# Optimization experiments

Measured on AMD Instinct MI355X. Metric: run time of the kernel, lower is better.

The kernel has to match this reference:

```python
import jax, jax.numpy as jnp
import numpy as np

N = 50000
D = 256
S = 25  # num_samples


def setup_inputs() -> dict:
    key = jax.random.key(0)
    ks = jax.random.split(key, 8)
    sc = 1.0 / np.sqrt(D)
    sc2 = 1.0 / np.sqrt(2 * D)
    return {
        "features": jax.random.normal(ks[0], (N, D), dtype=jnp.float32),
        "neigh_idx": jax.random.randint(ks[1], (N, S), 0, N, dtype=jnp.int64),
        "Wp0": jax.random.normal(ks[2], (D, D), dtype=jnp.float32) * sc,
        "bp0": jnp.zeros((D,), dtype=jnp.float32),
        "Wfc0": jax.random.normal(ks[3], (2 * D, D), dtype=jnp.float32) * sc2,
        "bfc0": jnp.zeros((D,), dtype=jnp.float32),
        "Wp1": jax.random.normal(ks[4], (D, D), dtype=jnp.float32) * sc,
        "bp1": jnp.zeros((D,), dtype=jnp.float32),
        "Wfc1": jax.random.normal(ks[5], (2 * D, D), dtype=jnp.float32) * sc2,
        "bfc1": jnp.zeros((D,), dtype=jnp.float32),
    }


def _sage_layer(out, neigh_idx, Wp, bp, Wfc, bfc):
    # MaxPoolAggregator: per-node Linear+ReLU on neighbor feats, then max-pool.
    # Transform once over all nodes, then gather (same math, less traffic).
    h = jax.nn.relu(out @ Wp + bp)          # [N, d]
    agg = jnp.max(h[neigh_idx], axis=1)     # gather [N, S, d] -> max -> [N, d]
    cat = jnp.concatenate([out, agg], axis=1)  # [N, 2d]
    return cat @ Wfc + bfc                  # [N, hidden]


def reference(features, neigh_idx, Wp0, bp0, Wfc0, bfc0, Wp1, bp1, Wfc1, bfc1):
    out = _sage_layer(features, neigh_idx, Wp0, bp0, Wfc0, bfc0)
    out = jax.nn.relu(out)  # relu between layers; dropout(p=0) is a no-op
    out = _sage_layer(out, neigh_idx, Wp1, bp1, Wfc1, bfc1)
    return out
```

## Files before the change

kernel.cpp:

```cpp
#include <hip/hip_runtime.h>
#include <stdint.h>

#define N_NODES 50000
#define DD 256
#define SS 25

typedef unsigned short u16;
typedef __attribute__((ext_vector_type(8))) __bf16 bf16x8;
typedef __attribute__((ext_vector_type(4))) float f32x4;

__device__ __forceinline__ u16 f2bf(float f) {
    union { float f; uint32_t i; } c;
    c.f = f;
    uint32_t r = c.i + 0x7fffu + ((c.i >> 16) & 1u);
    return (u16)(r >> 16);
}

__device__ __forceinline__ uint4 pkmax4(uint4 a, uint4 b) {
    uint4 d;
    asm("v_pk_max_i16 %0, %1, %2" : "=v"(d.x) : "v"(a.x), "v"(b.x));
    asm("v_pk_max_i16 %0, %1, %2" : "=v"(d.y) : "v"(a.y), "v"(b.y));
    asm("v_pk_max_i16 %0, %1, %2" : "=v"(d.z) : "v"(a.z), "v"(b.z));
    asm("v_pk_max_i16 %0, %1, %2" : "=v"(d.w) : "v"(a.w), "v"(b.w));
    return d;
}

__device__ __forceinline__ void gld16(void* lds, const void* g) {
    __builtin_amdgcn_global_load_lds(
        (const __attribute__((address_space(1))) uint32_t*)g,
        (__attribute__((address_space(3))) uint32_t*)lds, 16, 0, 0);
}

__global__ __launch_bounds__(256) void cvt_f32_bf16_k(const float4* __restrict__ in,
                                                      u16* __restrict__ out) {
    int i = blockIdx.x * 256 + threadIdx.x;
    float4 v = in[i];
    uint2 o;
    o.x = (uint32_t)f2bf(v.x) | ((uint32_t)f2bf(v.y) << 16);
    o.y = (uint32_t)f2bf(v.z) | ((uint32_t)f2bf(v.w) << 16);
    *reinterpret_cast<uint2*>(out + (size_t)i * 4) = o;
}

__global__ __launch_bounds__(256) void cvt_w_k(const float* __restrict__ W,
                                               u16* __restrict__ out, int KT) {
    int t = blockIdx.x * 256 + threadIdx.x;
    if (t >= KT * 16 * 64) return;
    int lane = t & 63;
    int ct = (t >> 6) & 15;
    int kt = t >> 10;
    int k0 = kt * 32 + (lane >> 4) * 8;
    int col = ct * 16 + (lane & 15);
    u16 r[8];
#pragma unroll
    for (int e = 0; e < 8; e++) r[e] = f2bf(W[(size_t)(k0 + e) * DD + col]);
    uint4 v;
    v.x = (uint32_t)r[0] | ((uint32_t)r[1] << 16);
    v.y = (uint32_t)r[2] | ((uint32_t)r[3] << 16);
    v.z = (uint32_t)r[4] | ((uint32_t)r[5] << 16);
    v.w = (uint32_t)r[6] | ((uint32_t)r[7] << 16);
    *reinterpret_cast<uint4*>(out + (size_t)t * 8) = v;
}

__global__ __launch_bounds__(256) void gather_xcd_k(const u16* __restrict__ hc,
                                                    const int* __restrict__ idx,
                                                    u16* __restrict__ aggc, int M) {
    const int c = blockIdx.x & 7;
    const int base = (blockIdx.x >> 3) * 256;
    __shared__ int soff[256 * SS];
    const int tid = threadIdx.x;
    for (int j = tid; j < 256 * SS; j += 256) {
        int n = base + j / SS;
        if (n >= M) n = M - 1;
        soff[j] = idx[(size_t)n * SS + (j % SS)] * 32;
    }
    __syncthreads();
    const int q = tid & 3;
    const u16* slice = hc + (size_t)c * ((size_t)N_NODES * 32) + q * 8;
    u16* aslice = aggc + (size_t)c * ((size_t)N_NODES * 32) + q * 8;
#pragma unroll 1
    for (int p = 0; p < 4; ++p) {
        const int slot = p * 64 + (tid >> 2);
        const int n = base + slot;
        const int* off = &soff[slot * SS];
        uint4 v[13];
#pragma unroll
        for (int s = 0; s < 13; ++s)
            v[s] = *reinterpret_cast<const uint4*>(slice + off[s]);
        uint4 run = v[0];
#pragma unroll
        for (int s = 1; s < 13; ++s) run = pkmax4(run, v[s]);
#pragma unroll
        for (int s = 13; s < 25; ++s)
            v[s - 13] = *reinterpret_cast<const uint4*>(slice + off[s]);
#pragma unroll
        for (int s = 0; s < 12; ++s) run = pkmax4(run, v[s]);
        if (n < M)
            *reinterpret_cast<uint4*>(aslice + (size_t)n * 32) = run;
    }
}

template <int KT, bool RELU, int OMODE>
__global__ __launch_bounds__(512, 4) void gemm_k(const u16* __restrict__ A1,
                                                 const u16* __restrict__ A2,
                                                 const u16* __restrict__ Bf,
                                                 const float* __restrict__ bias,
                                                 u16* __restrict__ obf,
                                                 float* __restrict__ of32, int M) {
    __shared__ u16 sA[4][4096];
    __shared__ u16 sB[3][8192];
    const int tid = threadIdx.x;
    const int lane = tid & 63, w = tid >> 6;
    const int wm = w >> 2, wn = w & 3;
    const int row_base = blockIdx.x * 128;
    const int lr = lane & 15, lk = lane >> 4;

    const int arow = tid >> 2;
    const int swzr = (arow + (arow >> 2)) & 3;
    const int kc = (tid & 3) ^ swzr;
    int sgrow = row_base + arow;
    if (sgrow >= M) sgrow = M - 1;

    auto stageB = [&](int buf, int kt) {
#pragma unroll
        for (int j = 0; j < 2; ++j) {
            const int idx = tid + j * 512;
            const int nl = idx >> 6, li = idx & 63;
            gld16(&sB[buf][idx * 8], Bf + ((size_t)(kt * 16 + nl) * 64 + li) * 8);
        }
    };
    auto stageA = [&](int buf, int kt) {
        const u16* srcA = (KT == 16 && kt >= 8)
                              ? A2 + ((size_t)(kt & 7) * N_NODES + sgrow) * 32 + kc * 8
                              : A1 + (size_t)sgrow * DD + (kt & 7) * 32 + kc * 8;
        gld16(&sA[buf][tid * 8], srcA);
    };

    f32x4 acc[4][4] = {};
    const int swzl = (lr + (lr >> 2)) & 3;
    auto compute = [&](int bufA, int bufB) {
        bf16x8 a[4], b[4];
#pragma unroll
        for (int m = 0; m < 4; m++) {
            const int row = wm * 64 + m * 16 + lr;
            a[m] = *reinterpret_cast<const bf16x8*>(
                &sA[bufA][(row * 4 + (lk ^ swzl)) * 8]);
        }
#pragma unroll
        for (int n = 0; n < 4; n++)
            b[n] = *reinterpret_cast<const bf16x8*>(
                &sB[bufB][((wn * 4 + n) * 64 + lane) * 8]);
#pragma unroll
        for (int m = 0; m < 4; m++)
#pragma unroll
            for (int n = 0; n < 4; n++)
                acc[m][n] = __builtin_amdgcn_mfma_f32_16x16x32_bf16(a[m], b[n], acc[m][n], 0, 0, 0);
    };

    stageB(0, 0);
    stageA(0, 0);
    stageB(1, 1);
    stageA(1, 1);
    stageA(2, 2);
#pragma unroll
    for (int kt = 0; kt < KT; ++kt) {
        if (kt < KT - 2)
            asm volatile("s_waitcnt vmcnt(4)" ::: "memory");
        else if (kt == KT - 2)
            asm volatile("s_waitcnt vmcnt(3)" ::: "memory");
        else
            asm volatile("s_waitcnt vmcnt(0)" ::: "memory");
        __builtin_amdgcn_s_barrier();
        if (kt + 2 < KT) stageB((kt + 2) % 3, kt + 2);
        if (kt + 3 < KT) stageA((kt + 3) & 3, kt + 3);
        compute(kt & 3, kt % 3);
    }

#pragma unroll
    for (int n = 0; n < 4; n++) {
        const int col = wn * 64 + n * 16 + lr;
        const float bz = bias[col];
#pragma unroll
        for (int m = 0; m < 4; m++) {
            const int r0 = row_base + wm * 64 + m * 16 + lk * 4;
#pragma unroll
            for (int e = 0; e < 4; e++) {
                const int r = r0 + e;
                if (r < M) {
                    float v = acc[m][n][e] + bz;
                    if (RELU) v = fmaxf(v, 0.0f);
                    if (OMODE == 0)
                        obf[(size_t)r * DD + col] = f2bf(v);
                    else if (OMODE == 1)
                        obf[((size_t)(col >> 5) * N_NODES + r) * 32 + (col & 31)] = f2bf(v);
                    else
                        of32[(size_t)r * DD + col] = v;
                }
            }
        }
    }
}

extern "C" void kernel_launch(void* const* d_in, const int* in_sizes, int n_in,
                              void* d_out, int out_size, void* d_ws, size_t ws_size,
                              hipStream_t stream) {
    const float* features = (const float*)d_in[0];
    const int* neigh = (const int*)d_in[1];
    const float* Wp0 = (const float*)d_in[2];
    const float* bp0 = (const float*)d_in[3];
    const float* Wfc0 = (const float*)d_in[4];
    const float* bfc0 = (const float*)d_in[5];
    const float* Wp1 = (const float*)d_in[6];
    const float* bp1 = (const float*)d_in[7];
    const float* Wfc1 = (const float*)d_in[8];
    const float* bfc1 = (const float*)d_in[9];
    float* out = (float*)d_out;

    const size_t ND = (size_t)N_NODES * DD;
    u16* B0 = (u16*)d_ws;
    u16* B1 = B0 + ND;
    u16* B2 = B1 + ND;
    u16* Wpb0 = B2 + ND;
    u16* Wfb0 = Wpb0 + 65536;
    u16* Wpb1 = Wfb0 + 131072;
    u16* Wfb1 = Wpb1 + 65536;

    cvt_w_k<<<32, 256, 0, stream>>>(Wp0, Wpb0, 8);
    cvt_w_k<<<64, 256, 0, stream>>>(Wfc0, Wfb0, 16);
    cvt_w_k<<<32, 256, 0, stream>>>(Wp1, Wpb1, 8);
    cvt_w_k<<<64, 256, 0, stream>>>(Wfc1, Wfb1, 16);
    cvt_f32_bf16_k<<<12500, 256, 0, stream>>>((const float4*)features, B0);

    const int gg = (N_NODES + 127) / 128;
    const int gx = ((N_NODES + 255) / 256) * 8;

    gemm_k<8, true, 1><<<gg, 512, 0, stream>>>(B0, nullptr, Wpb0, bp0, B1, nullptr, N_NODES);
    gather_xcd_k<<<gx, 256, 0, stream>>>(B1, neigh, B2, N_NODES);
    gemm_k<16, true, 0><<<gg, 512, 0, stream>>>(B0, B2, Wfb0, bfc0, B1, nullptr, N_NODES);

    gemm_k<8, true, 1><<<gg, 512, 0, stream>>>(B1, nullptr, Wpb1, bp1, B0, nullptr, N_NODES);
    gather_xcd_k<<<gx, 256, 0, stream>>>(B0, neigh, B2, N_NODES);
    gemm_k<16, false, 2><<<gg, 512, 0, stream>>>(B1, B2, Wfb1, bfc1, nullptr, out, N_NODES);
}
```

Baseline: 221.9 us.

## Fuse layer-0 FC GEMM with layer-1 pool projection GEMM in one kernel

Adds a kernel that computes the layer-0 concat FC (relu) for a 128-row tile, writes it to global, then immediately reuses the same block to compute the layer-1 pool projection from those rows. The intermediate is stored in the output buffer (bf16, column-blocked layout) to serve as the gather source. This removes one kernel launch and is meant to let the second GEMM re-read freshly written rows while they are still in cache. The trade-off is a longer kernel with reduced parallel overlap, and a read-after-write through global memory within the block that relies on a waitcnt and barrier for visibility.

```diff
diff --git a/kernel.cpp b/kernel.cpp
--- a/kernel.cpp
+++ b/kernel.cpp
@@ -200,6 +200,152 @@
     }
 }
 
+__global__ __launch_bounds__(512, 4) void fused2_k(const u16* __restrict__ X,
+                                                   const u16* __restrict__ agg0,
+                                                   const u16* __restrict__ BfT,
+                                                   const float* __restrict__ b0,
+                                                   u16* __restrict__ O0,
+                                                   const u16* __restrict__ Bp1,
+                                                   const float* __restrict__ b1,
+                                                   u16* __restrict__ h1c,
+                                                   int M) {
+    __shared__ u16 sA[4][4096];
+    __shared__ u16 sB[3][8192];
+    const int tid = threadIdx.x;
+    const int lane = tid & 63, w = tid >> 6;
+    const int wm = w >> 2, wn = w & 3;
+    const int row_base = blockIdx.x * 128;
+    const int lr = lane & 15, lk = lane >> 4;
+
+    const int arow = tid >> 2;
+    const int swzr = (arow + (arow >> 2)) & 3;
+    const int kc = (tid & 3) ^ swzr;
+    int sgrow = row_base + arow;
+    if (sgrow >= M) sgrow = M - 1;
+
+    const int swzl = (lr + (lr >> 2)) & 3;
+
+    auto stageB = [&](const u16* Bf, int buf, int kt) {
+#pragma unroll
+        for (int j = 0; j < 2; ++j) {
+            const int idx = tid + j * 512;
+            const int nl = idx >> 6, li = idx & 63;
+            gld16(&sB[buf][idx * 8], Bf + ((size_t)(kt * 16 + nl) * 64 + li) * 8);
+        }
+    };
+    auto stageA1 = [&](const u16* A1, int buf, int kt) {
+        gld16(&sA[buf][tid * 8], A1 + (size_t)sgrow * DD + (kt & 7) * 32 + kc * 8);
+    };
+    auto stageA2 = [&](const u16* A2, int buf, int kt) {
+        gld16(&sA[buf][tid * 8], A2 + ((size_t)(kt & 7) * N_NODES + sgrow) * 32 + kc * 8);
+    };
+
+    f32x4 acc[4][4] = {};
+    auto compute = [&](int bufA, int bufB) {
+        bf16x8 a[4], b[4];
+#pragma unroll
+        for (int m = 0; m < 4; m++) {
+            const int row = wm * 64 + m * 16 + lr;
+            a[m] = *reinterpret_cast<const bf16x8*>(
+                &sA[bufA][(row * 4 + (lk ^ swzl)) * 8]);
+        }
+#pragma unroll
+        for (int n = 0; n < 4; n++)
+            b[n] = *reinterpret_cast<const bf16x8*>(
+                &sB[bufB][((wn * 4 + n) * 64 + lane) * 8]);
+#pragma unroll
+        for (int m = 0; m < 4; m++)
+#pragma unroll
+            for (int n = 0; n < 4; n++)
+                acc[m][n] = __builtin_amdgcn_mfma_f32_16x16x32_bf16(a[m], b[n], acc[m][n], 0, 0, 0);
+    };
+
+    stageB(BfT, 0, 0);
+    stageA1(X, 0, 0);
+    stageB(BfT, 1, 1);
+    stageA1(X, 1, 1);
+    stageA1(X, 2, 2);
+#pragma unroll
+    for (int kt = 0; kt < 16; ++kt) {
+        if (kt < 14)
+            asm volatile("s_waitcnt vmcnt(4)" ::: "memory");
+        else if (kt == 14)
+            asm volatile("s_waitcnt vmcnt(3)" ::: "memory");
+        else
+            asm volatile("s_waitcnt vmcnt(0)" ::: "memory");
+        __builtin_amdgcn_s_barrier();
+        if (kt + 2 < 16) stageB(BfT, (kt + 2) % 3, kt + 2);
+        if (kt + 3 < 16) {
+            if (kt + 3 < 8)
+                stageA1(X, (kt + 3) & 3, kt + 3);
+            else
+                stageA2(agg0, (kt + 3) & 3, kt + 3);
+        }
+        compute(kt & 3, kt % 3);
+    }
+
+#pragma unroll
+    for (int n = 0; n < 4; n++) {
+        const int col = wn * 64 + n * 16 + lr;
+        const float bz = b0[col];
+#pragma unroll
+        for (int m = 0; m < 4; m++) {
+            const int r0 = row_base + wm * 64 + m * 16 + lk * 4;
+#pragma unroll
+            for (int e = 0; e < 4; e++) {
+                const int r = r0 + e;
+                if (r < M) O0[(size_t)r * DD + col] = f2bf(fmaxf(acc[m][n][e] + bz, 0.0f));
+            }
+        }
+    }
+    asm volatile("s_waitcnt vmcnt(0)" ::: "memory");
+    __builtin_amdgcn_s_barrier();
+
+#pragma unroll
+    for (int m = 0; m < 4; m++)
+#pragma unroll
+        for (int n = 0; n < 4; n++) acc[m][n] = f32x4{0.f, 0.f, 0.f, 0.f};
+
+    stageB(Bp1, 0, 0);
+    stageB(Bp1, 1, 1);
+    stageA1(O0, 0, 0);
+    stageA1(O0, 1, 1);
+    stageA1(O0, 2, 2);
+#pragma unroll
+    for (int kt = 0; kt < 8; ++kt) {
+        if (kt == 0)
+            asm volatile("s_waitcnt vmcnt(2)" ::: "memory");
+        else if (kt < 6)
+            asm volatile("s_waitcnt vmcnt(4)" ::: "memory");
+        else if (kt == 6)
+            asm volatile("s_waitcnt vmcnt(3)" ::: "memory");
+        else
+            asm volatile("s_waitcnt vmcnt(0)" ::: "memory");
+        __builtin_amdgcn_s_barrier();
+        if (kt + 2 < 8) stageB(Bp1, (kt + 2) % 3, kt + 2);
+        if (kt + 3 < 8) stageA1(O0, (kt + 3) & 3, kt + 3);
+        compute(kt & 3, kt % 3);
+    }
+
+#pragma unroll
+    for (int n = 0; n < 4; n++) {
+        const int col = wn * 64 + n * 16 + lr;
+        const float bz = b1[col];
+#pragma unroll
+        for (int m = 0; m < 4; m++) {
+            const int r0 = row_base + wm * 64 + m * 16 + lk * 4;
+#pragma unroll
+            for (int e = 0; e < 4; e++) {
+                const int r = r0 + e;
+                if (r < M) {
+                    float v = fmaxf(acc[m][n][e] + bz, 0.0f);
+                    h1c[((size_t)(col >> 5) * N_NODES + r) * 32 + (col & 31)] = f2bf(v);
+                }
+            }
+        }
+    }
+}
+
 extern "C" void kernel_launch(void* const* d_in, const int* in_sizes, int n_in,
                               void* d_out, int out_size, void* d_ws, size_t ws_size,
                               hipStream_t stream) {
@@ -223,6 +369,7 @@
     u16* Wfb0 = Wpb0 + 65536;
     u16* Wpb1 = Wfb0 + 131072;
     u16* Wfb1 = Wpb1 + 65536;
+    u16* H1 = (u16*)d_out;
 
     cvt_w_k<<<32, 256, 0, stream>>>(Wp0, Wpb0, 8);
     cvt_w_k<<<64, 256, 0, stream>>>(Wfc0, Wfb0, 16);
@@ -235,9 +382,8 @@
 
     gemm_k<8, true, 1><<<gg, 512, 0, stream>>>(B0, nullptr, Wpb0, bp0, B1, nullptr, N_NODES);
     gather_xcd_k<<<gx, 256, 0, stream>>>(B1, neigh, B2, N_NODES);
-    gemm_k<16, true, 0><<<gg, 512, 0, stream>>>(B0, B2, Wfb0, bfc0, B1, nullptr, N_NODES);
-
-    gemm_k<8, true, 1><<<gg, 512, 0, stream>>>(B1, nullptr, Wpb1, bp1, B0, nullptr, N_NODES);
-    gather_xcd_k<<<gx, 256, 0, stream>>>(B0, neigh, B2, N_NODES);
+    fused2_k<<<gg, 512, 0, stream>>>(B0, B2, Wfb0, bfc0, B1, Wpb1, bp1, H1, N_NODES);
+
+    gather_xcd_k<<<gx, 256, 0, stream>>>(H1, neigh, B2, N_NODES);
     gemm_k<16, false, 2><<<gg, 512, 0, stream>>>(B1, B2, Wfb1, bfc1, nullptr, out, N_NODES);
 }
```

After: 234.7 us. 5.8% more time.
